# Kernel tuning notes

Measured on AMD Instinct MI355X. Metric: run time of the kernel, lower is better.

## Reference

```python
import jax, jax.numpy as jnp
import numpy as np

VOCAB = 100000   # word_dim
RAND = 100       # random_dim
WAE = 50         # wae_dim
CLS = 4          # class_num
VDIM = 100       # _args.vocab_dim (WAE encoder embedding width)
P, L = 16384, 50 # num_paths, path_len


def setup_inputs() -> dict:
    key = jax.random.key(0)
    ks = jax.random.split(key, 6)
    x = jax.random.randint(ks[0], (P, L), 0, VOCAB)
    y = jnp.zeros((CLS,), jnp.int32).at[2].set(1)  # one-hot label
    E_td = 0.1 * jax.random.normal(ks[1], (VOCAB, RAND), jnp.float32)
    E_wae = 0.1 * jax.random.normal(ks[2], (VOCAB, VDIM), jnp.float32)
    W_enc = 0.1 * jax.random.normal(ks[3], (VDIM, WAE), jnp.float32)
    b_enc = jnp.zeros((WAE,), jnp.float32)
    w_out = 0.1 * jax.random.normal(ks[4], (CLS, RAND + WAE), jnp.float32)
    b_out = 0.1 * jax.random.normal(ks[5], (CLS,), jnp.float32)
    return dict(x=x, y=y, E_td=E_td, E_wae=E_wae, W_enc=W_enc,
                b_enc=b_enc, w_out=w_out, b_out=b_out)


def reference(x, y, E_td, E_wae, W_enc, b_enc, w_out, b_out):
    # path_random: embedding gather + sum over path tokens -> [P, RAND]
    path_random = E_td[x].sum(axis=1)
    # WAE encoder: bag-of-words embedding sum -> linear -> relu -> [P, WAE]
    bow = E_wae[x].sum(axis=1)
    path_wae = jax.nn.relu(bow @ W_enc + b_enc)
    # concat, leaky_relu (dropout is identity in eval mode)
    h = jax.nn.leaky_relu(jnp.concatenate([path_random, path_wae], axis=-1),
                          negative_slope=0.01)
    # max-pool over the path dimension -> [RAND+WAE]
    path_max = h.max(axis=0)
    # manual linear: elementwise mul + sum, bias add -> [CLS]
    logits = (w_out * path_max).sum(axis=1) + b_out
    prob = jax.nn.softmax(logits, axis=-1)
    # CrossEntropyLoss applied to the softmax output (as in the original)
    label = jnp.argmax(y)
    loss = -jax.nn.log_softmax(prob, axis=-1)[label]
    return prob, loss
```

## Files before the change

### kernel.cpp

```cpp
#include <hip/hip_runtime.h>


#define NPATH 16384
#define PLEN  50
#define RANDD 100
#define VDIMD 100
#define WAED  50
#define NCLS  4
#define HD    150
#define NTOK  100000
#define NBLK   1024
#define NBLK_M 683
#define NBLKC  391

#define QSCALE_TD 0.0048818898f
#define QINV_TD   204.83871f
#define QSCALE_F  0.0055118110f
#define QINV_F    181.42857f

__device__ __forceinline__ unsigned f2o(float f) {
    unsigned u = __float_as_uint(f);
    return (u & 0x80000000u) ? ~u : (u | 0x80000000u);
}
__device__ __forceinline__ float o2f(unsigned u) {
    return (u & 0x80000000u) ? __uint_as_float(u & 0x7FFFFFFFu)
                             : __uint_as_float(~u);
}

__device__ __forceinline__ unsigned q4(float4 v) {
    int q0 = (int)rintf(fminf(fmaxf(v.x * QINV_TD, -127.f), 127.f));
    int q1 = (int)rintf(fminf(fmaxf(v.y * QINV_TD, -127.f), 127.f));
    int q2 = (int)rintf(fminf(fmaxf(v.z * QINV_TD, -127.f), 127.f));
    int q3 = (int)rintf(fminf(fmaxf(v.w * QINV_TD, -127.f), 127.f));
    return (unsigned)(q0 & 0xff) | ((unsigned)(q1 & 0xff) << 8) |
           ((unsigned)(q2 & 0xff) << 16) | ((unsigned)(q3 & 0xff) << 24);
}

__device__ __forceinline__ int qb(float f) {
    return (int)rintf(fminf(fmaxf(f * QINV_F, -127.f), 127.f)) & 0xff;
}

__global__ void __launch_bounds__(256, 4)
convert_fold8(const float* __restrict__ E_td,
              const float* __restrict__ E_wae,
              const float* __restrict__ W_enc,
              unsigned char* __restrict__ T8,
              unsigned int* __restrict__ gmax)
{
    const int tid  = threadIdx.x;
    if (blockIdx.x == 0 && tid < HD + 10) gmax[tid] = 0u;
    const int lane = tid & 63;
    const int warp = tid >> 6;
    const int base = (blockIdx.x * 4 + warp) * 64;
    if (base >= NTOK) return;
    const int nt = (NTOK - base < 64) ? (NTOK - base) : 64;

    {
        const float* src = E_td + (size_t)base * RANDD;
        unsigned char* dstb = T8 + (size_t)base * 160;
        #pragma unroll 5
        for (int k = 0; k < 25; ++k) {
            int j = k * 64 + lane;
            int t = j / 25;
            if (t < nt) {
                float4 v = *(const float4*)(src + j * 4);
                *(unsigned*)(dstb + j * 4 + t * 60) = q4(v);
            }
        }
    }

    const bool pv  = (lane < nt);
    const int  tok = base + (pv ? lane : 0);
    const float* er = E_wae + (size_t)tok * VDIMD;

    float acc[WAED];
    #pragma unroll
    for (int d = 0; d < WAED; ++d) acc[d] = 0.f;

    for (int i4 = 0; i4 < 25; ++i4) {
        const float4 e = *(const float4*)(er + i4 * 4);
        const float* wr = W_enc + i4 * 4 * WAED;
        #pragma unroll
        for (int d = 0; d < WAED; ++d) {
            float a = acc[d];
            a = fmaf(e.x, wr[d],            a);
            a = fmaf(e.y, wr[WAED + d],     a);
            a = fmaf(e.z, wr[2 * WAED + d], a);
            a = fmaf(e.w, wr[3 * WAED + d], a);
            acc[d] = a;
        }
    }

    if (pv) {
        unsigned char* row = T8 + (size_t)tok * 160;
        #pragma unroll
        for (int k = 0; k < 12; ++k) {
            unsigned p = (unsigned)qb(acc[4 * k + 0])
                       | ((unsigned)qb(acc[4 * k + 1]) << 8)
                       | ((unsigned)qb(acc[4 * k + 2]) << 16)
                       | ((unsigned)qb(acc[4 * k + 3]) << 24);
            *(unsigned*)(row + 100 + 4 * k) = p;
        }
        *(unsigned*)(row + 148) = (unsigned)qb(acc[48])
                                | ((unsigned)qb(acc[49]) << 8);
        *(unsigned long long*)(row + 152) = 0ull;
    }
}

__global__ void __launch_bounds__(256, 4)
pathwae_main8(const int* __restrict__ x,
              const unsigned char* __restrict__ T8,
              const float* __restrict__ b_enc,
              unsigned int* __restrict__ gmax)
{
    __shared__ unsigned sh_bmax[HD + 10];
    __shared__ float    sh_benc[WAED];

    const int tid  = threadIdx.x;
    const int lane = tid & 63;
    const int warp = tid >> 6;
    if (tid < HD + 10) sh_bmax[tid] = 0u;
    if (tid < WAED)    sh_benc[tid] = b_enc[tid];
    __syncthreads();

    const int g   = lane / 10;
    const int sub = lane - g * 10;
    const int path = (blockIdx.x * 4 + warp) * 6 + g;
    const bool pvalid = (g < 6) && (path < NPATH);

    unsigned accE[4] = {0u,0u,0u,0u}, accO[4] = {0u,0u,0u,0u};

    if (pvalid) {
        int tokReg[5];
        #pragma unroll
        for (int k = 0; k < 5; ++k)
            tokReg[k] = x[path * PLEN + k * 10 + sub];
        const char* Tc = (const char*)T8;
        const unsigned qoff = (unsigned)(sub << 4);
        const int gl = g * 10;
        #pragma unroll 10
        for (int l = 0; l < PLEN; ++l) {
            int tok = __shfl(tokReg[l / 10], gl + (l % 10));
            uint4 q = *(const uint4*)(Tc + (unsigned)tok * 160u + qoff);
            const unsigned* wd = (const unsigned*)&q;
            #pragma unroll
            for (int j = 0; j < 4; ++j) {
                unsigned b = wd[j] ^ 0x80808080u;
                accE[j] += (b & 0x00FF00FFu);
                accO[j] += ((b >> 8) & 0x00FF00FFu);
            }
        }
    }

    const int srcA = ((g + 3) % 6) * 10 + sub;
    const int srcB = ((g + 1) % 6) * 10 + sub;
    const int srcC = ((g + 2) % 6) * 10 + sub;

    #pragma unroll
    for (int j = 0; j < 4; ++j) {
        const int ss[4] = { (int)(accE[j] & 0xFFFFu) - 6400,
                            (int)(accO[j] & 0xFFFFu) - 6400,
                            (int)(accE[j] >> 16)     - 6400,
                            (int)(accO[j] >> 16)     - 6400 };
        #pragma unroll
        for (int c = 0; c < 4; ++c) {
            const int dd = sub * 16 + j * 4 + c;
            float v;
            if (dd < RANDD) {
                float t = QSCALE_TD * (float)ss[c];
                v = t > 0.f ? t : 0.01f * t;
            } else if (dd < HD) {
                float t = fmaf(QSCALE_F, (float)ss[c], sh_benc[dd - RANDD]);
                v = fmaxf(t, 0.f);
            } else {
                v = -3.4e38f;
            }
            v = pvalid ? v : -3.4e38f;
            v = fmaxf(v, __shfl(v, srcA));
            v = fmaxf(v, __shfl(v, srcB));
            v = fmaxf(v, __shfl(v, srcC));
            if (g == 0 && dd < HD)
                atomicMax(&sh_bmax[dd], f2o(v));
        }
    }
    __syncthreads();
    if (tid < HD) atomicMax(&gmax[tid], sh_bmax[tid]);
}

__global__ void __launch_bounds__(256)
pathwae_final(const unsigned int* __restrict__ gmax,
              const int* __restrict__ y,
              const float* __restrict__ w_out,
              const float* __restrict__ b_out,
              float* __restrict__ out)
{
    __shared__ float pm[HD];
    __shared__ float lg[NCLS];
    const int tid = threadIdx.x;
    if (tid < HD) pm[tid] = o2f(gmax[tid]);
    __syncthreads();
    if (tid < NCLS) {
        float s = b_out[tid];
        for (int d = 0; d < HD; ++d)
            s = fmaf(w_out[tid * HD + d], pm[d], s);
        lg[tid] = s;
    }
    __syncthreads();
    if (tid == 0) {
        int label = 0, best = y[0];
        for (int c = 1; c < NCLS; ++c)
            if (y[c] > best) { best = y[c]; label = c; }
        float m = lg[0];
        for (int c = 1; c < NCLS; ++c) m = fmaxf(m, lg[c]);
        float e[NCLS], s = 0.f;
        for (int c = 0; c < NCLS; ++c) { e[c] = expf(lg[c] - m); s += e[c]; }
        float prob[NCLS];
        for (int c = 0; c < NCLS; ++c) prob[c] = e[c] / s;
        float m2 = prob[0];
        for (int c = 1; c < NCLS; ++c) m2 = fmaxf(m2, prob[c]);
        float s2 = 0.f;
        for (int c = 0; c < NCLS; ++c) s2 += expf(prob[c] - m2);
        float lse = m2 + logf(s2);
        for (int c = 0; c < NCLS; ++c) out[c] = prob[c];
        out[NCLS] = -(prob[label] - lse);
    }
}

__global__ void __launch_bounds__(256)
pathwae_main_f32(const int* __restrict__ x,
                 const float* __restrict__ E_td,
                 const float* __restrict__ E_wae,
                 const float* __restrict__ W_enc,
                 const float* __restrict__ b_enc,
                 unsigned int* __restrict__ gmax)
{
    __shared__ float sh_W[VDIMD * WAED];
    __shared__ float sh_bow[4][VDIMD];
    __shared__ float sh_wmax[4][HD];
    const int tid = threadIdx.x, lane = tid & 63, warp = tid >> 6;
    for (int i = tid; i < VDIMD * WAED; i += 256) sh_W[i] = W_enc[i];
    __syncthreads();
    const int gwave = blockIdx.x * 4 + warp, nwave = NBLK * 4;
    const bool is_td = (lane < 25), active = (lane < 50);
    const int chunk = is_td ? lane : (lane - 25);
    const float* tab = is_td ? E_td : E_wae;
    float4 maxtd = make_float4(-3.4e38f, -3.4e38f, -3.4e38f, -3.4e38f);
    float maxwae = -3.4e38f;
    const float benc = (lane < WAED) ? b_enc[lane] : 0.0f;
    for (int p = gwave; p < NPATH; p += nwave) {
        int mytok = (lane < PLEN) ? x[p * PLEN + lane] : 0;
        float ax = 0.f, ay = 0.f, az = 0.f, aw = 0.f;
        #pragma unroll 10
        for (int l = 0; l < PLEN; ++l) {
            int tok = __shfl(mytok, l);
            if (active) {
                float4 v = *(const float4*)(tab + tok * 100 + chunk * 4);
                ax += v.x; ay += v.y; az += v.z; aw += v.w;
            }
        }
        if (active && !is_td) {
            float* dst = &sh_bow[warp][chunk * 4];
            dst[0] = ax; dst[1] = ay; dst[2] = az; dst[3] = aw;
        }
        if (lane < WAED) {
            float w = benc;
            #pragma unroll 10
            for (int i = 0; i < VDIMD; ++i)
                w = fmaf(sh_bow[warp][i], sh_W[i * WAED + lane], w);
            w = fmaxf(w, 0.0f);
            maxwae = fmaxf(maxwae, w);
        }
        if (is_td) {
            maxtd.x = fmaxf(maxtd.x, ax > 0.f ? ax : 0.01f * ax);
            maxtd.y = fmaxf(maxtd.y, ay > 0.f ? ay : 0.01f * ay);
            maxtd.z = fmaxf(maxtd.z, az > 0.f ? az : 0.01f * az);
            maxtd.w = fmaxf(maxtd.w, aw > 0.f ? aw : 0.01f * aw);
        }
    }
    if (is_td) {
        sh_wmax[warp][chunk * 4 + 0] = maxtd.x;
        sh_wmax[warp][chunk * 4 + 1] = maxtd.y;
        sh_wmax[warp][chunk * 4 + 2] = maxtd.z;
        sh_wmax[warp][chunk * 4 + 3] = maxtd.w;
    }
    if (lane < WAED) sh_wmax[warp][RANDD + lane] = maxwae;
    __syncthreads();
    if (tid < HD) {
        float m = fmaxf(fmaxf(sh_wmax[0][tid], sh_wmax[1][tid]),
                        fmaxf(sh_wmax[2][tid], sh_wmax[3][tid]));
        atomicMax(&gmax[tid], f2o(m));
    }
}

extern "C" void kernel_launch(void* const* d_in, const int* in_sizes, int n_in,
                              void* d_out, int out_size, void* d_ws, size_t ws_size,
                              hipStream_t stream) {
    const int* x       = (const int*)d_in[0];
    const int* y       = (const int*)d_in[1];
    const float* E_td  = (const float*)d_in[2];
    const float* E_wae = (const float*)d_in[3];
    const float* W_enc = (const float*)d_in[4];
    const float* b_enc = (const float*)d_in[5];
    const float* w_out = (const float*)d_in[6];
    const float* b_out = (const float*)d_in[7];
    float* out         = (float*)d_out;

    unsigned int* gmax = (unsigned int*)d_ws;
    unsigned char* T8  = (unsigned char*)d_ws + 1024;
    const size_t need = 1024 + (size_t)NTOK * 160 + 256;

    if (ws_size >= need) {
        convert_fold8<<<NBLKC, 256, 0, stream>>>(E_td, E_wae, W_enc, T8, gmax);
        pathwae_main8<<<NBLK_M, 256, 0, stream>>>(x, T8, b_enc, gmax);
    } else {
        hipMemsetAsync(gmax, 0, HD * sizeof(unsigned int), stream);
        pathwae_main_f32<<<NBLK, 256, 0, stream>>>(x, E_td, E_wae, W_enc,
                                                   b_enc, gmax);
    }
    pathwae_final<<<1, 256, 0, stream>>>(gmax, y, w_out, b_out, out);
}
```

Baseline: 198.2 us.

## Split WAE fold across four warps per 64-token tile via LDS-transposed embeddings

The token-table conversion kernel now assigns one block per 64 tokens instead of four. It stages the E_wae rows transposed into shared memory, and each of the four warps computes about 13 of the 50 encoder outputs, instead of one lane computing all 50. This cuts per-thread accumulator registers from 50 to 13 and quadruples the grid. It adds a block barrier and 26 KB of LDS per block, and the output is now written as single bytes, with warps 2 and 3 overlapping at columns 37-38.

```diff
diff --git a/kernel.cpp b/kernel.cpp
--- a/kernel.cpp
+++ b/kernel.cpp
@@ -11,7 +11,7 @@
 #define NTOK  100000
 #define NBLK   1024
 #define NBLK_M 683
-#define NBLKC  391
+#define NBLKC  1563
 
 #define QSCALE_TD 0.0048818898f
 #define QINV_TD   204.83871f
@@ -40,70 +40,74 @@
     return (int)rintf(fminf(fmaxf(f * QINV_F, -127.f), 127.f)) & 0xff;
 }
 
-__global__ void __launch_bounds__(256, 4)
+__global__ void __launch_bounds__(256)
 convert_fold8(const float* __restrict__ E_td,
               const float* __restrict__ E_wae,
               const float* __restrict__ W_enc,
               unsigned char* __restrict__ T8,
               unsigned int* __restrict__ gmax)
 {
-    const int tid  = threadIdx.x;
+    __shared__ float sh_eT[VDIMD * 65];
+
+    const int tid = threadIdx.x;
     if (blockIdx.x == 0 && tid < HD + 10) gmax[tid] = 0u;
-    const int lane = tid & 63;
-    const int warp = tid >> 6;
-    const int base = (blockIdx.x * 4 + warp) * 64;
-    if (base >= NTOK) return;
-    const int nt = (NTOK - base < 64) ? (NTOK - base) : 64;
+
+    const int base = blockIdx.x * 64;
+    const int nt   = (NTOK - base < 64) ? (NTOK - base) : 64;
+
+    for (int k = tid; k < nt * 25; k += 256) {
+        const int t = k / 25;
+        const int c = k - t * 25;
+        float4 v = *(const float4*)(E_wae + (size_t)(base + t) * VDIMD + c * 4);
+        const int i = c * 4;
+        sh_eT[(i    ) * 65 + t] = v.x;
+        sh_eT[(i + 1) * 65 + t] = v.y;
+        sh_eT[(i + 2) * 65 + t] = v.z;
+        sh_eT[(i + 3) * 65 + t] = v.w;
+    }
 
     {
         const float* src = E_td + (size_t)base * RANDD;
         unsigned char* dstb = T8 + (size_t)base * 160;
-        #pragma unroll 5
-        for (int k = 0; k < 25; ++k) {
-            int j = k * 64 + lane;
-            int t = j / 25;
-            if (t < nt) {
-                float4 v = *(const float4*)(src + j * 4);
-                *(unsigned*)(dstb + j * 4 + t * 60) = q4(v);
-            }
-        }
-    }
-
-    const bool pv  = (lane < nt);
-    const int  tok = base + (pv ? lane : 0);
-    const float* er = E_wae + (size_t)tok * VDIMD;
-
-    float acc[WAED];
+        for (int k = tid; k < nt * 25; k += 256) {
+            const int t = k / 25;
+            float4 v = *(const float4*)(src + k * 4);
+            *(unsigned*)(dstb + k * 4 + t * 60) = q4(v);
+        }
+    }
+    __syncthreads();
+
+    const int lane = tid & 63;
+    const int q  = __builtin_amdgcn_readfirstlane(tid >> 6);
+    const int dq = (q == 3) ? 37 : q * 13;
+
+    float acc[13];
     #pragma unroll
-    for (int d = 0; d < WAED; ++d) acc[d] = 0.f;
-
-    for (int i4 = 0; i4 < 25; ++i4) {
-        const float4 e = *(const float4*)(er + i4 * 4);
-        const float* wr = W_enc + i4 * 4 * WAED;
+    for (int j = 0; j < 13; ++j) acc[j] = 0.f;
+
+    const float* Wq = W_enc + dq;
+    #pragma unroll 4
+    for (int i = 0; i < VDIMD; ++i) {
+        const float e = sh_eT[i * 65 + lane];
+        const float* w = Wq + i * WAED;
         #pragma unroll
-        for (int d = 0; d < WAED; ++d) {
-            float a = acc[d];
-            a = fmaf(e.x, wr[d],            a);
-            a = fmaf(e.y, wr[WAED + d],     a);
-            a = fmaf(e.z, wr[2 * WAED + d], a);
-            a = fmaf(e.w, wr[3 * WAED + d], a);
-            acc[d] = a;
-        }
-    }
-
-    if (pv) {
-        unsigned char* row = T8 + (size_t)tok * 160;
-        #pragma unroll
-        for (int k = 0; k < 12; ++k) {
-            unsigned p = (unsigned)qb(acc[4 * k + 0])
-                       | ((unsigned)qb(acc[4 * k + 1]) << 8)
-                       | ((unsigned)qb(acc[4 * k + 2]) << 16)
-                       | ((unsigned)qb(acc[4 * k + 3]) << 24);
-            *(unsigned*)(row + 100 + 4 * k) = p;
-        }
-        *(unsigned*)(row + 148) = (unsigned)qb(acc[48])
-                                | ((unsigned)qb(acc[49]) << 8);
-        *(unsigned long long*)(row + 152) = 0ull;
+        for (int j = 0; j < 13; ++j)
+            acc[j] = fmaf(e, w[j], acc[j]);
+    }
+
+    if (lane < nt) {
+        unsigned char* row = T8 + (size_t)(base + lane) * 160;
+        if (q == 3) {
+            #pragma unroll
+            for (int j = 2; j < 13; ++j)
+                row[100 + dq + j] = (unsigned char)qb(acc[j]);
+            *(unsigned short*)(row + 150) = 0;
+            *(unsigned long long*)(row + 152) = 0ull;
+        } else {
+            #pragma unroll
+            for (int j = 0; j < 13; ++j)
+                row[100 + dq + j] = (unsigned char)qb(acc[j]);
+        }
     }
 }
 
```

Result: faster. 188.9 us (-4.7%).
